# Optimization experiments

Measured on AMD Instinct MI355X. Metric: run time of the kernel, lower is better.

Reference implementation:

```python
import jax, jax.numpy as jnp
from jax import lax
import numpy as np

B, T, U, P, K = 8192, 256, 64, 64, 2048

def setup_inputs() -> dict:
    key = jax.random.key(0)
    ku, ky, kw1, kw2 = jax.random.split(key, 4)
    u = jax.random.normal(ku, (B, T, U), dtype=jnp.float32)
    y0 = jax.random.normal(ky, (B, P), dtype=jnp.float32)
    W1 = jax.random.normal(kw1, (U + P, K), dtype=jnp.float32) * (1.0 / np.sqrt(U + P))
    b1 = jnp.zeros((K,), dtype=jnp.float32)
    W2 = jax.random.normal(kw2, (K, 1), dtype=jnp.float32) * (1.0 / np.sqrt(K))
    b2 = jnp.zeros((1,), dtype=jnp.float32)
    return {"u": u, "y0": y0, "W1": W1, "b1": b1, "W2": W2, "b2": b2}

def reference(u, y0, W1, b1, W2, b2):
    def step(y, u_t):
        # x: [B, U+P]
        x = jnp.concatenate([u_t, y], axis=1)
        h = jnp.tanh(x @ W1 + b1)          # [B, K]
        pred = h @ W2 + b2                 # [B, 1]
        # roll(shift=1)[:,1:] == y[:, :-1]; newest prediction goes to front
        y_new = jnp.concatenate([pred, y[:, :-1]], axis=1)  # [B, P]
        return y_new, pred

    u_t_first = jnp.swapaxes(u, 0, 1)      # [T, B, U]
    _, preds = lax.scan(step, y0, u_t_first)  # preds: [T, B, 1]
    return jnp.transpose(preds, (1, 0, 2))    # [B, T, 1]
```

## Files before the change

kernel.cpp:

```cpp
#include <hip/hip_runtime.h>
#include <hip/hip_fp16.h>
#include <cstdint>
#include <cstddef>

#define T_STEPS 256
#define K_DIM 2048
#define NCW 8
#define NT_W 8
#define REG_NT 4
#define LDS_NT 4

typedef _Float16 f16;
typedef _Float16 f16x8 __attribute__((ext_vector_type(8)));
typedef _Float16 f16x4 __attribute__((ext_vector_type(4)));
typedef float f32x4 __attribute__((ext_vector_type(4)));

#define W1S_OFF 0
#define U_OFF   131072
#define Y_OFF   139264
#define PB_OFF  155648
#define CS_OFF  156672
#define SMEM_BYTES 156928

#define W1P_BYTES (128 * 4 * 64 * 16)
#define MBOX_OFF  W1P_BYTES
#define MBOX_BYTES (256 * 2 * 2 * 32 * 8)

__global__ void __launch_bounds__(64) prepack_w1(const float* __restrict__ W1,
                                                 f16* __restrict__ w1p) {
  int blk = blockIdx.x;
  int ntile = blk >> 2, ks = blk & 3;
  int lane = threadIdx.x;
  int col = ntile * 16 + (lane & 15);
  int kb = ks * 32 + ((lane >> 4) << 3);
  f16x8 pk;
#pragma unroll
  for (int i = 0; i < 8; ++i) pk[i] = (f16)W1[(size_t)(kb + i) * K_DIM + col];
  ((f16x8*)w1p)[(ntile * 4 + ks) * 64 + lane] = pk;
}

__global__ void __launch_bounds__(512, 2)
__attribute__((amdgpu_waves_per_eu(2, 2)))
rnn_fused(const float* __restrict__ u, const float* __restrict__ y0,
          const f16* __restrict__ w1p, const float* __restrict__ b1,
          const float* __restrict__ w2, const float* __restrict__ b2,
          float* __restrict__ out, unsigned long long* mbox)
{
  __shared__ __align__(16) char smem[SMEM_BYTES];
  f16x8* w1s     = (f16x8*)(smem + W1S_OFF);
  float* predbuf = (float*)(smem + PB_OFF);
  float* cslot   = (float*)(smem + CS_OFF);

  const int tid = threadIdx.x, lane = tid & 63, wave = tid >> 6;
  const int b = blockIdx.x;
  const int jj_ = b >> 3;
  const int half = jj_ & 1;
  const int pair = ((b & 7) << 4) | (jj_ >> 1);
  const int partner = b ^ 8;
  const int row0 = pair * 64;
  const int colbase = half * 1024;
  const float b2v = b2[0];
  const f16x8* w1pv = (const f16x8*)w1p;
  const float TWO_L = 2.885390081777927f;

  float b1x[NT_W], w2v[NT_W];
#pragma unroll
  for (int nt = 0; nt < NT_W; ++nt) {
    int col = colbase + wave * 128 + nt * 16 + (lane & 15);
    b1x[nt] = TWO_L * b1[col];
    w2v[nt] = w2[col];
  }

  float Chalf = 0.f;
  if (wave == 0) {
    float s = 0.f;
#pragma unroll
    for (int i = 0; i < 16; ++i) s += w2[colbase + lane * 16 + i];
    s += __shfl_xor(s, 1);  s += __shfl_xor(s, 2);  s += __shfl_xor(s, 4);
    s += __shfl_xor(s, 8);  s += __shfl_xor(s, 16); s += __shfl_xor(s, 32);
    Chalf = s;
  }

  f16x8 w1r[REG_NT * 4];
#pragma unroll
  for (int nt = 0; nt < REG_NT; ++nt)
#pragma unroll
    for (int ks = 0; ks < 4; ++ks)
      w1r[nt * 4 + ks] = w1pv[((half * 64 + wave * 8 + nt) * 4 + ks) * 64 + lane];
#pragma unroll
  for (int i = 0; i < REG_NT * 4; ++i) asm volatile("" : "+v"(w1r[i]));
#pragma unroll
  for (int nt = 0; nt < LDS_NT; ++nt)
#pragma unroll
    for (int ks = 0; ks < 4; ++ks)
      w1s[((wave * LDS_NT + nt) * 4 + ks) * 64 + lane] =
          w1pv[((half * 64 + wave * 8 + REG_NT + nt) * 4 + ks) * 64 + lane];

  const int r_i = tid >> 4;
  const int j0c = (tid & 15) * 4;
  const int sw_i = (r_i & 7) << 4;
  float4 upA, upB;
#pragma unroll
  for (int g = 0; g < 2; ++g) {
    int row = row0 + g * 32 + r_i;
    {
      float4 a = *(const float4*)(y0 + (size_t)row * 64 + j0c);
      f16x4 pk; pk[0] = (f16)a.x; pk[1] = (f16)a.y; pk[2] = (f16)a.z; pk[3] = (f16)a.w;
      *(f16x4*)(smem + Y_OFF + (g * 2 + 0) * 4096 + ((r_i * 128 + j0c * 2) ^ sw_i)) = pk;
    }
    {
      float4 a = *(const float4*)(u + ((size_t)row * T_STEPS + 0) * 64 + j0c);
      f16x4 pk; pk[0] = (f16)a.x; pk[1] = (f16)a.y; pk[2] = (f16)a.z; pk[3] = (f16)a.w;
      *(f16x4*)(smem + U_OFF + g * 4096 + ((r_i * 128 + j0c * 2) ^ sw_i)) = pk;
    }
    float4 p1 = *(const float4*)(u + ((size_t)row * T_STEPS + 1) * 64 + j0c);
    if (g == 0) upA = p1; else upB = p1;
  }
  __syncthreads();

  float contrib1 = 0.f;

  auto phase = [&](int g, int t) {
    const int par = t & 1;
    const char* ubase = smem + U_OFF + g * 4096;
    const char* ybase = smem + Y_OFF + (g * 2 + par) * 4096;

    const int gp = g ^ 1;
    const bool pub = (wave == 1) && (lane < 32) && ((g == 1) || (t > 0));
    const unsigned want = (g == 0) ? (unsigned)t : (unsigned)(t + 1);
    const int slot = (g == 0) ? ((t - 1) & 1) : (t & 1);
    const unsigned long long* mb =
        &mbox[((size_t)((partner * 2 + gp) * 2 + slot)) * 32 + lane];
    unsigned long long pv0 = 0;
    if (pub) {
      pv0 = __hip_atomic_load(mb, __ATOMIC_RELAXED, __HIP_MEMORY_SCOPE_AGENT);
      asm volatile("" : "+v"(pv0));
    }

    f16x8 af[2][4];
    {
      int koff = (lane >> 4) << 4;
#pragma unroll
      for (int mt = 0; mt < 2; ++mt) {
        int r = mt * 16 + (lane & 15);
        int base = r * 128 + koff, sw = (r & 7) << 4;
        af[mt][0] = *(const f16x8*)(ubase + (base ^ sw));
        af[mt][1] = *(const f16x8*)(ubase + ((base + 64) ^ sw));
        af[mt][2] = *(const f16x8*)(ybase + (base ^ sw));
        af[mt][3] = *(const f16x8*)(ybase + ((base + 64) ^ sw));
      }
    }

    auto mfma_nt = [&](int nt, f32x4* acc) {
      acc[0] = (f32x4){0.f, 0.f, 0.f, 0.f};
      acc[1] = (f32x4){0.f, 0.f, 0.f, 0.f};
      __builtin_amdgcn_s_setprio(1);
#pragma unroll
      for (int ks = 0; ks < 4; ++ks) {
        f16x8 bf = (nt < REG_NT)
                       ? w1r[nt * 4 + ks]
                       : w1s[((wave * LDS_NT + (nt - REG_NT)) * 4 + ks) * 64 + lane];
        acc[0] = __builtin_amdgcn_mfma_f32_16x16x32_f16(af[0][ks], bf, acc[0], 0, 0, 0);
        acc[1] = __builtin_amdgcn_mfma_f32_16x16x32_f16(af[1][ks], bf, acc[1], 0, 0, 0);
      }
      __builtin_amdgcn_s_setprio(0);
    };

    float predp[2][4];
#pragma unroll
    for (int mt = 0; mt < 2; ++mt)
#pragma unroll
      for (int jj = 0; jj < 4; ++jj) predp[mt][jj] = 0.f;

    auto epi = [&](int nt, f32x4* acc) {
#pragma unroll
      for (int mt = 0; mt < 2; ++mt)
#pragma unroll
        for (int jj = 0; jj < 4; ++jj) {
          float e  = __builtin_amdgcn_exp2f(fmaf(TWO_L, acc[mt][jj], b1x[nt]));
          float rr = __builtin_amdgcn_rcpf(1.0f + e);
          predp[mt][jj] = fmaf(w2v[nt], rr, predp[mt][jj]);
        }
    };

    f32x4 accA[2], accB[2];
    mfma_nt(0, accA);
    mfma_nt(1, accB);
    epi(0, accA); mfma_nt(2, accA);
    epi(1, accB); mfma_nt(3, accB);
    epi(2, accA); mfma_nt(4, accA);
    epi(3, accB); mfma_nt(5, accB);
    epi(4, accA); mfma_nt(6, accA);
    epi(5, accB); mfma_nt(7, accB);
    epi(6, accA);
    epi(7, accB);

#pragma unroll
    for (int mt = 0; mt < 2; ++mt)
#pragma unroll
      for (int jj = 0; jj < 4; ++jj) {
        float v = predp[mt][jj];
        v += __shfl_xor(v, 1); v += __shfl_xor(v, 2);
        v += __shfl_xor(v, 4); v += __shfl_xor(v, 8);
        if ((lane & 15) == 0)
          predbuf[wave * 32 + mt * 16 + ((lane >> 4) << 2) + jj] = v;
      }

    if (pub) {
      unsigned long long pv = pv0;
      while ((unsigned)(pv >> 32) != want)
        pv = __hip_atomic_load(mb, __ATOMIC_RELAXED, __HIP_MEMORY_SCOPE_AGENT);
      float pc = __builtin_bit_cast(float, (unsigned)(pv & 0xffffffffu));
      float ps = cslot[gp * 32 + lane] + pc + b2v;
      const int pubpar = (g == 0) ? (t & 1) : ((t + 1) & 1);
      const int outcol = (g == 0) ? (t - 1) : t;
      *(f16*)(smem + Y_OFF + (gp * 2 + pubpar) * 4096 +
              ((lane * 128) ^ ((lane & 7) << 4))) = (f16)ps;
      if (half == 0)
        out[(size_t)(row0 + gp * 32 + lane) * T_STEPS + outcol] = ps;
    }
    __syncthreads();

    if (wave == 0 && lane < 32) {
      float own = 0.f;
#pragma unroll
      for (int w = 0; w < NCW; ++w) own += predbuf[w * 32 + lane];
      float c = fmaf(-2.0f, own, Chalf);
      if (g == 1) contrib1 = c;
      cslot[g * 32 + lane] = c;
      unsigned long long val =
          ((unsigned long long)(unsigned)(t + 1) << 32) |
          (unsigned long long)__builtin_bit_cast(unsigned, c);
      __hip_atomic_store(&mbox[((size_t)((b * 2 + g) * 2 + par)) * 32 + lane], val,
                         __ATOMIC_RELAXED, __HIP_MEMORY_SCOPE_AGENT);
    }

    {
      const char* yp = smem + Y_OFF + (g * 2 + par) * 4096;
      char*       yn = smem + Y_OFF + (g * 2 + (par ^ 1)) * 4096;
      f16x4 chB = *(const f16x4*)(yp + ((r_i * 128 + j0c * 2) ^ sw_i));
      f16x4 nw;
      nw[0] = j0c ? *(const f16*)(yp + ((r_i * 128 + j0c * 2 - 2) ^ sw_i)) : (f16)0.f;
      nw[1] = chB[0]; nw[2] = chB[1]; nw[3] = chB[2];
      *(f16x4*)(yn + ((r_i * 128 + j0c * 2) ^ sw_i)) = nw;

      if (t + 1 < T_STEPS) {
        float4 up = (g == 0) ? upA : upB;
        f16x4 pk; pk[0] = (f16)up.x; pk[1] = (f16)up.y; pk[2] = (f16)up.z; pk[3] = (f16)up.w;
        *(f16x4*)(smem + U_OFF + g * 4096 + ((r_i * 128 + j0c * 2) ^ sw_i)) = pk;
      }
      if (t + 2 < T_STEPS) {
        float4 p = *(const float4*)(
            u + ((size_t)(row0 + g * 32 + r_i) * T_STEPS + (t + 2)) * 64 + j0c);
        if (g == 0) upA = p; else upB = p;
      }
    }
    __syncthreads();
  };

  for (int t = 0; t < T_STEPS; ++t) {
    phase(0, t);
    phase(1, t);
  }

  if (wave == 0 && lane < 32) {
    const unsigned want = (unsigned)T_STEPS;
    unsigned long long pv;
    const unsigned long long* mb =
        &mbox[((size_t)((partner * 2 + 1) * 2 + 1)) * 32 + lane];
    do {
      pv = __hip_atomic_load(mb, __ATOMIC_RELAXED, __HIP_MEMORY_SCOPE_AGENT);
    } while ((unsigned)(pv >> 32) != want);
    float pc = __builtin_bit_cast(float, (unsigned)(pv & 0xffffffffu));
    float ps = contrib1 + pc + b2v;
    if (half == 0)
      out[(size_t)(row0 + 32 + lane) * T_STEPS + (T_STEPS - 1)] = ps;
  }
}

extern "C" void kernel_launch(void* const* d_in, const int* in_sizes, int n_in,
                              void* d_out, int out_size, void* d_ws, size_t ws_size,
                              hipStream_t stream) {
  const float* u  = (const float*)d_in[0];
  const float* y0 = (const float*)d_in[1];
  const float* W1 = (const float*)d_in[2];
  const float* b1 = (const float*)d_in[3];
  const float* W2 = (const float*)d_in[4];
  const float* b2 = (const float*)d_in[5];

  f16* w1p = (f16*)d_ws;
  unsigned long long* mbox = (unsigned long long*)((char*)d_ws + MBOX_OFF);

  hipMemsetAsync((char*)d_ws + MBOX_OFF, 0, MBOX_BYTES, stream);

  prepack_w1<<<512, 64, 0, stream>>>(W1, w1p);

  rnn_fused<<<256, 512, 0, stream>>>(u, y0, w1p, b1, W2, b2, (float*)d_out, mbox);
}
```

Measured before the change: 1.996 ms.

## Merge cross-block reduction and shift into next group's region, one barrier per phase

Restructures each half-step so the reduction of the previous group's partial predictions, the mailbox publish, the y-shift and the u prefetch for the other row group happen at the start of the next region, before its MFMA work. This removes one __syncthreads per phase, and the partner-block wait is overlapped with the matrix work. predbuf is double-buffered per group and the cslot buffer is replaced by registers. The cost is more LDS usage and a restructured ordering that must keep the y buffer parity correct.

```diff
diff --git a/kernel.cpp b/kernel.cpp
--- a/kernel.cpp
+++ b/kernel.cpp
@@ -13,14 +13,14 @@
 typedef _Float16 f16;
 typedef _Float16 f16x8 __attribute__((ext_vector_type(8)));
 typedef _Float16 f16x4 __attribute__((ext_vector_type(4)));
+typedef _Float16 f16x2 __attribute__((ext_vector_type(2)));
 typedef float f32x4 __attribute__((ext_vector_type(4)));
 
 #define W1S_OFF 0
 #define U_OFF   131072
 #define Y_OFF   139264
 #define PB_OFF  155648
-#define CS_OFF  156672
-#define SMEM_BYTES 156928
+#define SMEM_BYTES 157696
 
 #define W1P_BYTES (128 * 4 * 64 * 16)
 #define MBOX_OFF  W1P_BYTES
@@ -49,7 +49,6 @@
   __shared__ __align__(16) char smem[SMEM_BYTES];
   f16x8* w1s     = (f16x8*)(smem + W1S_OFF);
   float* predbuf = (float*)(smem + PB_OFF);
-  float* cslot   = (float*)(smem + CS_OFF);
 
   const int tid = threadIdx.x, lane = tid & 63, wave = tid >> 6;
   const int b = blockIdx.x;
@@ -118,25 +117,63 @@
   }
   __syncthreads();
 
-  float contrib1 = 0.f;
-
-  auto phase = [&](int g, int t) {
+  float contrib0 = 0.f, contrib1 = 0.f;
+
+  auto region = [&](int g, int t) {
+    const int gp = g ^ 1;
+    const int t_p = (g == 1) ? t : t - 1;
     const int par = t & 1;
+    const int par_p = t_p & 1;
+
+    unsigned long long pv0 = 0;
+    const unsigned long long* mb = nullptr;
+
+    if (t_p >= 0) {
+      if (wave == 0 && lane < 32) {
+        float own = 0.f;
+#pragma unroll
+        for (int w = 0; w < NCW; ++w) own += predbuf[gp * 256 + w * 32 + lane];
+        float c = fmaf(-2.0f, own, Chalf);
+        if (gp == 0) contrib0 = c; else contrib1 = c;
+        unsigned long long val =
+            ((unsigned long long)(unsigned)(t_p + 1) << 32) |
+            (unsigned long long)__builtin_bit_cast(unsigned, c);
+        __hip_atomic_store(&mbox[((size_t)((b * 2 + gp) * 2 + par_p)) * 32 + lane], val,
+                           __ATOMIC_RELAXED, __HIP_MEMORY_SCOPE_AGENT);
+        mb = &mbox[((size_t)((partner * 2 + gp) * 2 + par_p)) * 32 + lane];
+        pv0 = __hip_atomic_load(mb, __ATOMIC_RELAXED, __HIP_MEMORY_SCOPE_AGENT);
+        asm volatile("" : "+v"(pv0));
+      }
+      {
+        const char* yp = smem + Y_OFF + (gp * 2 + par_p) * 4096;
+        char*       yn = smem + Y_OFF + (gp * 2 + (par_p ^ 1)) * 4096;
+        f16x4 chB = *(const f16x4*)(yp + ((r_i * 128 + j0c * 2) ^ sw_i));
+        char* dst = yn + ((r_i * 128 + j0c * 2) ^ sw_i);
+        if (j0c) {
+          f16x4 nw;
+          nw[0] = *(const f16*)(yp + ((r_i * 128 + j0c * 2 - 2) ^ sw_i));
+          nw[1] = chB[0]; nw[2] = chB[1]; nw[3] = chB[2];
+          *(f16x4*)dst = nw;
+        } else {
+          *(f16*)(dst + 2) = chB[0];
+          f16x2 hi; hi[0] = chB[1]; hi[1] = chB[2];
+          *(f16x2*)(dst + 4) = hi;
+        }
+        if (t_p + 1 < T_STEPS) {
+          float4 up = (gp == 0) ? upA : upB;
+          f16x4 pk; pk[0] = (f16)up.x; pk[1] = (f16)up.y; pk[2] = (f16)up.z; pk[3] = (f16)up.w;
+          *(f16x4*)(smem + U_OFF + gp * 4096 + ((r_i * 128 + j0c * 2) ^ sw_i)) = pk;
+        }
+        if (t_p + 2 < T_STEPS) {
+          float4 p = *(const float4*)(
+              u + ((size_t)(row0 + gp * 32 + r_i) * T_STEPS + (t_p + 2)) * 64 + j0c);
+          if (gp == 0) upA = p; else upB = p;
+        }
+      }
+    }
+
     const char* ubase = smem + U_OFF + g * 4096;
     const char* ybase = smem + Y_OFF + (g * 2 + par) * 4096;
-
-    const int gp = g ^ 1;
-    const bool pub = (wave == 1) && (lane < 32) && ((g == 1) || (t > 0));
-    const unsigned want = (g == 0) ? (unsigned)t : (unsigned)(t + 1);
-    const int slot = (g == 0) ? ((t - 1) & 1) : (t & 1);
-    const unsigned long long* mb =
-        &mbox[((size_t)((partner * 2 + gp) * 2 + slot)) * 32 + lane];
-    unsigned long long pv0 = 0;
-    if (pub) {
-      pv0 = __hip_atomic_load(mb, __ATOMIC_RELAXED, __HIP_MEMORY_SCOPE_AGENT);
-      asm volatile("" : "+v"(pv0));
-    }
-
     f16x8 af[2][4];
     {
       int koff = (lane >> 4) << 4;
@@ -203,67 +240,40 @@
         v += __shfl_xor(v, 1); v += __shfl_xor(v, 2);
         v += __shfl_xor(v, 4); v += __shfl_xor(v, 8);
         if ((lane & 15) == 0)
-          predbuf[wave * 32 + mt * 16 + ((lane >> 4) << 2) + jj] = v;
-      }
-
-    if (pub) {
+          predbuf[g * 256 + wave * 32 + mt * 16 + ((lane >> 4) << 2) + jj] = v;
+      }
+
+    if (t_p >= 0 && wave == 0 && lane < 32) {
+      const unsigned want = (unsigned)(t_p + 1);
       unsigned long long pv = pv0;
       while ((unsigned)(pv >> 32) != want)
         pv = __hip_atomic_load(mb, __ATOMIC_RELAXED, __HIP_MEMORY_SCOPE_AGENT);
       float pc = __builtin_bit_cast(float, (unsigned)(pv & 0xffffffffu));
-      float ps = cslot[gp * 32 + lane] + pc + b2v;
-      const int pubpar = (g == 0) ? (t & 1) : ((t + 1) & 1);
-      const int outcol = (g == 0) ? (t - 1) : t;
-      *(f16*)(smem + Y_OFF + (gp * 2 + pubpar) * 4096 +
-              ((lane * 128) ^ ((lane & 7) << 4))) = (f16)ps;
+      float ps = ((gp == 0) ? contrib0 : contrib1) + pc + b2v;
+      if (t_p + 1 < T_STEPS)
+        *(f16*)(smem + Y_OFF + (gp * 2 + ((t_p + 1) & 1)) * 4096 +
+                ((lane * 128) ^ ((lane & 7) << 4))) = (f16)ps;
       if (half == 0)
-        out[(size_t)(row0 + gp * 32 + lane) * T_STEPS + outcol] = ps;
-    }
-    __syncthreads();
-
-    if (wave == 0 && lane < 32) {
-      float own = 0.f;
-#pragma unroll
-      for (int w = 0; w < NCW; ++w) own += predbuf[w * 32 + lane];
-      float c = fmaf(-2.0f, own, Chalf);
-      if (g == 1) contrib1 = c;
-      cslot[g * 32 + lane] = c;
-      unsigned long long val =
-          ((unsigned long long)(unsigned)(t + 1) << 32) |
-          (unsigned long long)__builtin_bit_cast(unsigned, c);
-      __hip_atomic_store(&mbox[((size_t)((b * 2 + g) * 2 + par)) * 32 + lane], val,
-                         __ATOMIC_RELAXED, __HIP_MEMORY_SCOPE_AGENT);
-    }
-
-    {
-      const char* yp = smem + Y_OFF + (g * 2 + par) * 4096;
-      char*       yn = smem + Y_OFF + (g * 2 + (par ^ 1)) * 4096;
-      f16x4 chB = *(const f16x4*)(yp + ((r_i * 128 + j0c * 2) ^ sw_i));
-      f16x4 nw;
-      nw[0] = j0c ? *(const f16*)(yp + ((r_i * 128 + j0c * 2 - 2) ^ sw_i)) : (f16)0.f;
-      nw[1] = chB[0]; nw[2] = chB[1]; nw[3] = chB[2];
-      *(f16x4*)(yn + ((r_i * 128 + j0c * 2) ^ sw_i)) = nw;
-
-      if (t + 1 < T_STEPS) {
-        float4 up = (g == 0) ? upA : upB;
-        f16x4 pk; pk[0] = (f16)up.x; pk[1] = (f16)up.y; pk[2] = (f16)up.z; pk[3] = (f16)up.w;
-        *(f16x4*)(smem + U_OFF + g * 4096 + ((r_i * 128 + j0c * 2) ^ sw_i)) = pk;
-      }
-      if (t + 2 < T_STEPS) {
-        float4 p = *(const float4*)(
-            u + ((size_t)(row0 + g * 32 + r_i) * T_STEPS + (t + 2)) * 64 + j0c);
-        if (g == 0) upA = p; else upB = p;
-      }
+        out[(size_t)(row0 + gp * 32 + lane) * T_STEPS + t_p] = ps;
     }
     __syncthreads();
   };
 
   for (int t = 0; t < T_STEPS; ++t) {
-    phase(0, t);
-    phase(1, t);
+    region(0, t);
+    region(1, t);
   }
 
   if (wave == 0 && lane < 32) {
+    float own = 0.f;
+#pragma unroll
+    for (int w = 0; w < NCW; ++w) own += predbuf[1 * 256 + w * 32 + lane];
+    float c1 = fmaf(-2.0f, own, Chalf);
+    unsigned long long val =
+        ((unsigned long long)(unsigned)T_STEPS << 32) |
+        (unsigned long long)__builtin_bit_cast(unsigned, c1);
+    __hip_atomic_store(&mbox[((size_t)((b * 2 + 1) * 2 + 1)) * 32 + lane], val,
+                       __ATOMIC_RELAXED, __HIP_MEMORY_SCOPE_AGENT);
     const unsigned want = (unsigned)T_STEPS;
     unsigned long long pv;
     const unsigned long long* mb =
@@ -272,7 +282,7 @@
       pv = __hip_atomic_load(mb, __ATOMIC_RELAXED, __HIP_MEMORY_SCOPE_AGENT);
     } while ((unsigned)(pv >> 32) != want);
     float pc = __builtin_bit_cast(float, (unsigned)(pv & 0xffffffffu));
-    float ps = contrib1 + pc + b2v;
+    float ps = c1 + pc + b2v;
     if (half == 0)
       out[(size_t)(row0 + 32 + lane) * T_STEPS + (T_STEPS - 1)] = ps;
   }
```

New measurement: 1.834 ms. 8.1% less time.
